# Kernel optimization log

Measured on AMD Instinct MI355X. Metric: run time of the kernel, lower is better.

Reference implementation:

```python
import jax, jax.numpy as jnp
import numpy as np

S, B, C, H, W = 5, 2, 128, 24, 24
N_ITER = 3
BN_EPS = 1e-5


def conv2d(x, w, b, pad):
    # x: (N, Cin, H, W), w: (Cout, Cin, kh, kw)
    y = jax.lax.conv_general_dilated(
        x, w, (1, 1), [(pad, pad), (pad, pad)],
        dimension_numbers=('NCHW', 'OIHW', 'NCHW'))
    return y + b[None, :, None, None]


def setup_inputs() -> dict:
    key = jax.random.key(0)
    ks = jax.random.split(key, 8)
    sc = 0.03  # keep pre-softmax logits in a sane range
    d = {}
    d['x'] = jax.random.normal(ks[0], (S, B, C, H, W), jnp.float32) * 0.5
    d['Wf_w'] = jax.random.normal(ks[1], (C, C, 3, 3), jnp.float32) * sc
    d['Wf_b'] = jnp.zeros((C,), jnp.float32)
    d['Wh_w'] = jax.random.normal(ks[2], (C, C, 3, 3), jnp.float32) * sc
    d['Wh_b'] = jnp.zeros((C,), jnp.float32)
    d['Wl_w'] = jax.random.normal(ks[3], (C, C, 3, 3), jnp.float32) * sc
    d['Wl_b'] = jnp.zeros((C,), jnp.float32)
    d['alpha'] = jnp.ones((1,), jnp.float32)
    d['Wc'] = jax.random.normal(ks[4], (C, C), jnp.float32) * sc
    d['Wg_w'] = jax.random.normal(ks[5], (C, C, 3, 3), jnp.float32) * sc
    d['Wg_b'] = jnp.zeros((C,), jnp.float32)
    d['bn_gamma'] = jnp.ones((C,), jnp.float32)
    d['bn_beta'] = jnp.zeros((C,), jnp.float32)
    d['gru_zr_w'] = jax.random.normal(ks[6], (2 * C, 2 * C, 5, 5), jnp.float32) * sc
    d['gru_zr_b'] = jnp.zeros((2 * C,), jnp.float32)
    d['gru_h_w'] = jax.random.normal(ks[7], (C, 2 * C, 5, 5), jnp.float32) * sc
    d['gru_h_b'] = jnp.zeros((C,), jnp.float32)
    d['intra_w'] = jnp.full((1,), 0.5, jnp.float32)
    d['inter_w'] = jnp.full((1,), 0.5, jnp.float32)
    return d


def reference(x, Wf_w, Wf_b, Wh_w, Wh_b, Wl_w, Wl_b, alpha, Wc, Wg_w, Wg_b,
              bn_gamma, bn_beta, gru_zr_w, gru_zr_b, gru_h_w, gru_h_b,
              intra_w, inter_w):
    S_, B_, C_, H_, W_ = x.shape
    N = H_ * W_
    # BatchNorm2d in inference mode with fresh running stats (mean=0, var=1)
    bn_scale = bn_gamma / jnp.sqrt(1.0 + BN_EPS)
    mask = (1.0 - jnp.eye(S_, dtype=x.dtype))[:, :, None, None, None, None]
    h = x
    for _ in range(N_ITER):
        hb = h.reshape(S_ * B_, C_, H_, W_)
        # ---- intra-node self-attention (per node in sequence) ----
        ft = conv2d(hb, Wf_w, Wf_b, 1).reshape(S_, B_, C_, N)
        ht = conv2d(hb, Wh_w, Wh_b, 1).reshape(S_, B_, C_, N)
        lt = conv2d(hb, Wl_w, Wl_b, 1).reshape(S_, B_, C_, N)
        att = jax.nn.softmax(jnp.einsum('sbcn,sbcm->sbnm', ft, ht), axis=-1)
        ctx = jnp.einsum('sbnm,sbcm->sbcn', att, lt).reshape(S_, B_, C_, H_, W_)
        eii = alpha[0] * ctx + h
        # ---- inter-node pairwise attention messages (all i,j pairs) ----
        hf = h.reshape(S_, B_, C_, N)
        yt = jnp.einsum('cd,jbdn->jbcn', Wc, hf)
        eij = jnp.einsum('ibcn,jbcm->ijbnm', hf, yt)  # (S,S,B,N,N)
        eijn = jax.nn.softmax(eij, axis=-1)
        mji = jnp.einsum('ijbnm,jbcm->ijbcn', eijn, hf)  # (S,S,B,C,N)
        m4 = mji.reshape(S_ * S_ * B_, C_, H_, W_)
        g = jax.nn.sigmoid(jnp.mean(conv2d(m4, Wg_w, Wg_b, 1),
                                    axis=(2, 3), keepdims=True))
        mg = (g * m4) * bn_scale[None, :, None, None] + bn_beta[None, :, None, None]
        mg = mg.reshape(S_, S_, B_, C_, H_, W_)
        inter = jnp.sum(mg * mask, axis=1)  # exclude j == i
        msg = intra_w[0] * eii + inter_w[0] * inter
        # ---- ConvGRU update + residual ----
        xi = msg.reshape(S_ * B_, C_, H_, W_)
        zr = jax.nn.sigmoid(conv2d(jnp.concatenate([xi, hb], axis=1),
                                   gru_zr_w, gru_zr_b, 2))
        z, r = zr[:, :C_], zr[:, C_:]
        h_hat = jnp.tanh(conv2d(jnp.concatenate([xi, r * hb], axis=1),
                                gru_h_w, gru_h_b, 2))
        h_new = (1.0 - z) * hb + z * h_hat
        h = (h_new + hb).reshape(S_, B_, C_, H_, W_)
    return h
```

## Files before the change

kernel.cpp:

```cpp
#include <hip/hip_runtime.h>
#include <math.h>

#define S_  5
#define B_  2
#define C_  128
#define N_  576
#define SB  10
#define NPAIR 40
#define C2  256

typedef short v8s __attribute__((ext_vector_type(8)));
typedef float v4f __attribute__((ext_vector_type(4)));

#define GLOBAL_AS __attribute__((address_space(1)))
#define LDS_AS    __attribute__((address_space(3)))

__device__ __forceinline__ unsigned short f2bf(float f) {
    union { float f; unsigned u; } v; v.f = f;
    unsigned r = (v.u + 0x7FFF + ((v.u >> 16) & 1)) >> 16;
    return (unsigned short)r;
}
__device__ __forceinline__ float bf2f(unsigned short h) {
    union { unsigned u; float f; } v; v.u = ((unsigned)h) << 16;
    return v.f;
}

__global__ void packA5_kernel(const float* __restrict__ w, unsigned short* __restrict__ Apk, int M)
{
    int idx = blockIdx.x * 256 + threadIdx.x;
    if (idx >= M * 6400) return;
    int r = idx;
    int j = r & 7;      r >>= 3;
    int quad = r & 3;   r >>= 2;
    int l15 = r & 15;   r >>= 4;
    int c = r & 3;      r >>= 2;
    int tap_l = r % 5;  r /= 5;
    int g = r % 5;      r /= 5;
    int ch = r & 1;     r >>= 1;
    int kk = r & 3;     r >>= 2;
    int cgb = r;
    int co = cgb * 64 + c * 16 + l15;
    int ci = kk * 64 + ch * 32 + quad * 8 + j;
    int tap = g * 5 + tap_l;
    Apk[idx] = f2bf(w[((size_t)co * 256 + ci) * 25 + tap]);
}
__global__ void packA3_kernel(const float* __restrict__ wf, const float* __restrict__ wh,
                              const float* __restrict__ wl, unsigned short* __restrict__ Apk)
{
    int idx = blockIdx.x * 256 + threadIdx.x;
    if (idx >= 384 * 1152) return;
    int r = idx;
    int j = r & 7;      r >>= 3;
    int quad = r & 3;   r >>= 2;
    int l15 = r & 15;   r >>= 4;
    int c = r & 3;      r >>= 2;
    int tap_l = r % 3;  r /= 3;
    int g = r % 3;      r /= 3;
    int ch = r & 1;     r >>= 1;
    int kk = r & 1;     r >>= 1;
    int cgb = r;
    int co = cgb * 64 + c * 16 + l15;
    const float* w = (co < 128) ? wf : (co < 256) ? wh : wl;
    int cl = co & 127;
    int ci = kk * 64 + ch * 32 + quad * 8 + j;
    int tap = g * 3 + tap_l;
    Apk[idx] = f2bf(w[((size_t)cl * 128 + ci) * 9 + tap]);
}
__global__ void packWc_kernel(const float* __restrict__ w, unsigned short* __restrict__ o)
{
    int idx = blockIdx.x * 256 + threadIdx.x;
    if (idx < 128 * 128) o[idx] = f2bf(w[idx]);
}
__global__ void packWgT_kernel(const float* __restrict__ w, float* __restrict__ o)
{
    int idx = blockIdx.x * 256 + threadIdx.x;
    if (idx >= 128 * 1152) return;
    int co = idx & 127, i = idx >> 7;
    o[(size_t)i * 128 + co] = w[(size_t)co * 1152 + i];
}

__global__ __launch_bounds__(256) void tc_kernel(
    const float* __restrict__ src, const float* __restrict__ zrp,
    const float* __restrict__ zrb,
    unsigned short* __restrict__ dst, unsigned short* __restrict__ vfd)
{
    const size_t PLANE = (size_t)SB * C2 * N_;
    __shared__ float tile[128][9];
    int img = blockIdx.y, px0 = blockIdx.x * 8, t = threadIdx.x;
    #pragma unroll
    for (int i = 0; i < 4; ++i) {
        int e = i * 256 + t; int ci = e >> 3; int px = e & 7;
        float v = src[((size_t)img * 128 + ci) * 576 + px0 + px];
        if (zrp) {
            size_t zi = ((size_t)img * C2 + 128 + ci) * 576 + px0 + px;
            float a = zrb[128 + ci];
            #pragma unroll
            for (int k = 0; k < 4; ++k) a += zrp[k * PLANE + zi];
            v *= 1.f / (1.f + __expf(-a));
        }
        tile[ci][px] = v;
        if (vfd) {
            int m = px0 + px;
            int ctile = ci >> 4, l15v = ci & 15;
            int sIdx = m >> 5, quadv = (m >> 3) & 3, j = m & 7;
            vfd[(((size_t)img * 8 + ctile) * 18 + sIdx) * 512 + (quadv * 16 + l15v) * 8 + j] = f2bf(v);
        }
    }
    __syncthreads();
    #pragma unroll
    for (int i = 0; i < 4; ++i) {
        int e = i * 256 + t; int pxl = e >> 7; int ci = e & 127;
        dst[((size_t)img * 576 + px0 + pxl) * 128 + ci] = f2bf(tile[ci][pxl]);
    }
}

template<int KD, int R, int CINT, int SPLITK, int MODE>
__global__ __launch_bounds__(256, 1) void conv_mfma(
    const unsigned short* __restrict__ srcA, const unsigned short* __restrict__ srcB,
    const unsigned short* __restrict__ Apk, int COUT, float* __restrict__ po,
    const float* __restrict__ b0, const float* __restrict__ b1, const float* __restrict__ b2,
    unsigned short* __restrict__ t0, unsigned short* __restrict__ t1,
    unsigned short* __restrict__ t2)
{
    constexpr int PART   = CINT / SPLITK;
    constexpr int NCH    = PART / 32;
    constexpr int NSUB   = NCH * KD;
    constexpr int WR     = 8 + 2 * R;
    constexpr int WC     = 24 + 2 * R;
    constexpr int NPOS   = WR * WC;
    constexpr int NSLOTB = NPOS * 4;
    constexpr int RB     = (NSLOTB + 255) / 256;
    constexpr int AUNITS = KD * 4 * 64;
    constexpr int AR     = AUNITS / 256;
    __shared__ __align__(16) unsigned short Ab[2][AUNITS * 8];
    __shared__ __align__(16) unsigned short Bb[NPOS * 32];

    int f   = blockIdx.x;
    int kk  = f % SPLITK;
    int cgb = f / SPLITK;
    int pxb = blockIdx.y;
    int img = blockIdx.z;
    int t = threadIdx.x;
    int wave = t >> 6, lane = t & 63;
    int quad = lane >> 4, l15 = lane & 15;
    int r0 = pxb * 8;

    const int cibase = kk * PART;
    const unsigned short* src = (cibase >= 128) ? srcB : srcA;
    const int cioff0 = cibase & 127;
    const unsigned short* srcI = src + (size_t)img * 576 * 128;

    int posBase[3], pxs[3];
    #pragma unroll
    for (int s = 0; s < 3; ++s) {
        int px = pxb * 192 + wave * 48 + s * 16 + l15;
        pxs[s] = px;
        int pr = px / 24, pc = px % 24;
        posBase[s] = (pr - r0 + R) * WC + pc + R;
    }

    int goffB[RB]; bool gokB[RB];
    #pragma unroll
    for (int rr = 0; rr < RB; ++rr) {
        int idx = rr * 256 + wave * 64 + lane;
        int pos = idx >> 2, slotq = idx & 3;
        int gr = slotq ^ ((pos >> 1) & 3);
        int wr = pos / WC, wc = pos % WC;
        int grow = r0 - R + wr, gcol = wc - R;
        gokB[rr] = (idx < NSLOTB) && grow >= 0 && grow < 24 && gcol >= 0 && gcol < 24;
        goffB[rr] = (grow * 24 + gcol) * 128 + gr * 8;
    }

    auto stageB = [&](int ch) {
        const unsigned short* sp = srcI + cioff0 + ch * 32;
        #pragma unroll
        for (int rr = 0; rr < RB; ++rr) {
            if (gokB[rr]) {
                __builtin_amdgcn_global_load_lds(
                    (const GLOBAL_AS void*)(sp + goffB[rr]),
                    (LDS_AS void*)((char*)&Bb[0] + (size_t)(rr * 256 + wave * 64) * 16),
                    16, 0, 0);
            }
        }
    };
    auto stageA = [&](int sub, int buf) {
        const unsigned short* sp = Apk + ((size_t)((cgb * SPLITK + kk) * NSUB + sub)) * (AUNITS * 8);
        #pragma unroll
        for (int r = 0; r < AR; ++r) {
            int u0 = r * 256 + wave * 64;
            __builtin_amdgcn_global_load_lds(
                (const GLOBAL_AS void*)(sp + (size_t)(u0 + lane) * 8),
                (LDS_AS void*)((char*)&Ab[buf][0] + (size_t)u0 * 16),
                16, 0, 0);
        }
    };

    v4f acc[4][3];
    #pragma unroll
    for (int c = 0; c < 4; ++c)
        #pragma unroll
        for (int s = 0; s < 3; ++s)
            #pragma unroll
            for (int r = 0; r < 4; ++r) acc[c][s][r] = 0.f;

    {
        v8s zv;
        #pragma unroll
        for (int j = 0; j < 8; ++j) zv[j] = 0;
        for (int i = t; i < NPOS * 4; i += 256) ((v8s*)Bb)[i] = zv;
    }
    __syncthreads();
    stageB(0);
    stageA(0, 0);
    __syncthreads();

    int sub = 0;
    #pragma unroll 1
    for (int ch = 0; ch < NCH; ++ch) {
        #pragma unroll 1
        for (int g = 0; g < KD; ++g) {
            if (sub + 1 < NSUB) stageA(sub + 1, (sub + 1) & 1);
            const unsigned short* Ap = &Ab[sub & 1][0];
            #pragma unroll
            for (int tl = 0; tl < KD; ++tl) {
                int doff = (g - R) * WC + (tl - R);
                v8s a[4];
                #pragma unroll
                for (int c = 0; c < 4; ++c)
                    a[c] = *(const v8s*)&Ap[((tl * 4 + c) * 64 + l15 * 4 + quad) * 8];
                v8s b[3];
                #pragma unroll
                for (int s = 0; s < 3; ++s) {
                    int pos = posBase[s] + doff;
                    b[s] = *(const v8s*)&Bb[pos * 32 + ((quad ^ ((pos >> 1) & 3)) << 3)];
                }
                #pragma unroll
                for (int c = 0; c < 4; ++c)
                    #pragma unroll
                    for (int s = 0; s < 3; ++s)
                        acc[c][s] = __builtin_amdgcn_mfma_f32_16x16x32_bf16(a[c], b[s], acc[c][s], 0, 0, 0);
            }
            __syncthreads();
            ++sub;
        }
        if (ch + 1 < NCH) { stageB(ch + 1); __syncthreads(); }
    }

    if (MODE == 0) {
        float* out = po + (size_t)kk * ((size_t)SB * COUT * 576)
                   + ((size_t)img * COUT + cgb * 64) * 576;
        #pragma unroll
        for (int c = 0; c < 4; ++c)
            #pragma unroll
            for (int s = 0; s < 3; ++s)
                #pragma unroll
                for (int r = 0; r < 4; ++r) {
                    int col = c * 16 + quad * 4 + r;
                    out[(size_t)col * 576 + pxs[s]] = acc[c][s][r];
                }
    } else {
        #pragma unroll
        for (int c = 0; c < 4; ++c)
            #pragma unroll
            for (int s = 0; s < 3; ++s) {
                int px = pxs[s];
                #pragma unroll
                for (int r = 0; r < 4; ++r) {
                    int co = cgb * 64 + c * 16 + quad * 4 + r;
                    int which = co >> 7, cl = co & 127;
                    const float* bp = (which == 0) ? b0 : (which == 1) ? b1 : b2;
                    float v = acc[c][s][r] + bp[cl];
                    if (which == 0) {
                        t0[((size_t)img * 576 + px) * 128 + cl] = f2bf(v);
                    } else if (which == 1) {
                        int mt = px >> 4, l15m = px & 15;
                        int kb = cl >> 5, quadk = (cl >> 3) & 3, jj = cl & 7;
                        t1[(((size_t)img * 36 + mt) * 4 + kb) * 512 + (quadk * 16 + l15m) * 8 + jj] = f2bf(v);
                    } else {
                        int ctile = cl >> 4, l15v = cl & 15;
                        int sIdx = px >> 5, quadv = (px >> 3) & 3, jj = px & 7;
                        t2[(((size_t)img * 8 + ctile) * 18 + sIdx) * 512 + (quadv * 16 + l15v) * 8 + jj] = f2bf(v);
                    }
                }
            }
    }
}

__global__ __launch_bounds__(256) void yt_mfma(
    const unsigned short* __restrict__ hT, const unsigned short* __restrict__ Wcb,
    unsigned short* __restrict__ KFi)
{
    int t = threadIdx.x, wave = t >> 6, lane = t & 63;
    int q = lane >> 4, l15 = lane & 15;
    int n0 = blockIdx.x * 16, img = blockIdx.y;
    v4f acc[2];
    #pragma unroll
    for (int ct = 0; ct < 2; ++ct)
        #pragma unroll
        for (int r = 0; r < 4; ++r) acc[ct][r] = 0.f;
    #pragma unroll
    for (int kk = 0; kk < 4; ++kk) {
        v8s b = *(const v8s*)(hT + ((size_t)img * 576 + n0 + l15) * 128 + kk * 32 + q * 8);
        #pragma unroll
        for (int ct = 0; ct < 2; ++ct) {
            v8s a = *(const v8s*)(Wcb + (size_t)((wave * 2 + ct) * 16 + l15) * 128 + kk * 32 + q * 8);
            acc[ct] = __builtin_amdgcn_mfma_f32_16x16x32_bf16(a, b, acc[ct], 0, 0, 0);
        }
    }
    int mt = blockIdx.x;
    #pragma unroll
    for (int ct = 0; ct < 2; ++ct) {
        #pragma unroll
        for (int r = 0; r < 4; ++r) {
            int co = (wave * 2 + ct) * 16 + q * 4 + r;
            int kk = co >> 5, quadk = (co >> 3) & 3, j = co & 7;
            KFi[(((size_t)img * 36 + mt) * 4 + kk) * 512 + (quadk * 16 + l15) * 8 + j]
                = f2bf(acc[ct][r]);
        }
    }
}

template<int MODE>
__global__ __launch_bounds__(256) void attn_mfma(
    const unsigned short* __restrict__ QT, const unsigned short* __restrict__ KF,
    const unsigned short* __restrict__ VF, float* __restrict__ Of,
    unsigned short* __restrict__ Oh, const float* __restrict__ addsrc,
    const float* __restrict__ alpha)
{
    __shared__ __align__(16) unsigned short P[16 * 576];
    __shared__ float redmx[4][16];
    __shared__ float redsm[4][16];
    int t = threadIdx.x;
    int wave = t >> 6, lane = t & 63;
    int q = lane >> 4, l15 = lane & 15;
    int n0 = blockIdx.x * 16;
    int p = blockIdx.y;
    int qimg, kimg;
    if (MODE == 0) { qimg = p; kimg = p; }
    else {
        int b = p & 1; int ij = p >> 1; int i = ij >> 2; int jj = ij & 3;
        int j = jj + (jj >= i ? 1 : 0);
        qimg = i * 2 + b; kimg = j * 2 + b;
    }
    const unsigned short* Qp = QT + ((size_t)qimg * 576 + n0) * 128;
    const unsigned short* Kp = KF + (size_t)kimg * 36 * 4 * 512;
    const unsigned short* Vp = VF + (size_t)kimg * 8 * 18 * 512;

    v8s aq[4];
    #pragma unroll
    for (int kk = 0; kk < 4; ++kk)
        aq[kk] = *(const v8s*)(Qp + (size_t)l15 * 128 + kk * 32 + q * 8);

    v4f S[9];
    #pragma unroll
    for (int i = 0; i < 9; ++i)
        #pragma unroll
        for (int r = 0; r < 4; ++r) S[i][r] = 0.f;

    #pragma unroll
    for (int i = 0; i < 9; ++i) {
        int mt = wave * 9 + i;
        #pragma unroll
        for (int kk = 0; kk < 4; ++kk) {
            v8s b = *(const v8s*)(Kp + ((size_t)(mt * 4 + kk)) * 512 + lane * 8);
            S[i] = __builtin_amdgcn_mfma_f32_16x16x32_bf16(aq[kk], b, S[i], 0, 0, 0);
        }
    }

    float mx[4];
    #pragma unroll
    for (int r = 0; r < 4; ++r) {
        float m = S[0][r];
        #pragma unroll
        for (int i = 1; i < 9; ++i) m = fmaxf(m, S[i][r]);
        #pragma unroll
        for (int off = 1; off < 16; off <<= 1) m = fmaxf(m, __shfl_xor(m, off));
        mx[r] = m;
    }
    if (l15 == 0) {
        #pragma unroll
        for (int r = 0; r < 4; ++r) redmx[wave][q * 4 + r] = mx[r];
    }
    __syncthreads();
    float sum[4];
    #pragma unroll
    for (int r = 0; r < 4; ++r) {
        float g = fmaxf(fmaxf(redmx[0][q * 4 + r], redmx[1][q * 4 + r]),
                        fmaxf(redmx[2][q * 4 + r], redmx[3][q * 4 + r]));
        float s = 0.f;
        #pragma unroll
        for (int i = 0; i < 9; ++i) { float e = __expf(S[i][r] - g); S[i][r] = e; s += e; }
        #pragma unroll
        for (int off = 1; off < 16; off <<= 1) s += __shfl_xor(s, off);
        sum[r] = s;
    }
    if (l15 == 0) {
        #pragma unroll
        for (int r = 0; r < 4; ++r) redsm[wave][q * 4 + r] = sum[r];
    }
    #pragma unroll
    for (int i = 0; i < 9; ++i) {
        int m = (wave * 9 + i) * 16 + l15;
        int cm = m >> 3, mo = m & 7;
        #pragma unroll
        for (int r = 0; r < 4; ++r) {
            int n = q * 4 + r;
            P[n * 576 + ((cm ^ (n & 7)) << 3) + mo] = f2bf(S[i][r]);
        }
    }
    __syncthreads();
    float inv[4];
    #pragma unroll
    for (int r = 0; r < 4; ++r)
        inv[r] = 1.f / (redsm[0][q * 4 + r] + redsm[1][q * 4 + r] +
                        redsm[2][q * 4 + r] + redsm[3][q * 4 + r]);

    v4f o[2];
    #pragma unroll
    for (int ct = 0; ct < 2; ++ct)
        #pragma unroll
        for (int r = 0; r < 4; ++r) o[ct][r] = 0.f;

    for (int s = 0; s < 18; ++s) {
        int cm = s * 4 + q;
        v8s a = *(const v8s*)&P[l15 * 576 + ((cm ^ (l15 & 7)) << 3)];
        #pragma unroll
        for (int ct = 0; ct < 2; ++ct) {
            int ctile = wave * 2 + ct;
            v8s b = *(const v8s*)(Vp + ((size_t)(ctile * 18 + s)) * 512 + lane * 8);
            o[ct] = __builtin_amdgcn_mfma_f32_16x16x32_bf16(a, b, o[ct], 0, 0, 0);
        }
    }

    #pragma unroll
    for (int ct = 0; ct < 2; ++ct) {
        int c = (wave * 2 + ct) * 16 + l15;
        size_t base = ((size_t)p * 128 + c) * 576 + n0 + q * 4;
        if (MODE == 0) {
            float al = alpha[0];
            #pragma unroll
            for (int r = 0; r < 4; ++r)
                Of[base + r] = al * o[ct][r] * inv[r] + addsrc[base + r];
        } else {
            #pragma unroll
            for (int r = 0; r < 4; ++r)
                Oh[base + r] = f2bf(o[ct][r] * inv[r]);
        }
    }
}

__global__ __launch_bounds__(64) void wsum_kernel(
    const unsigned short* __restrict__ mji, float* __restrict__ wsum)
{
    int pair = blockIdx.x, ci = blockIdx.y, lane = threadIdx.x;
    const unsigned short* p = mji + ((size_t)pair * C_ + ci) * N_;
    float T=0, R0=0, R23=0, Cl=0, Cr=0, c00=0, c0w=0, ch0=0, chw=0;
    for (int i = lane; i < N_; i += 64) {
        float v = bf2f(p[i]);
        int r = i / 24, cc = i % 24;
        T += v;
        if (r == 0)  R0  += v;
        if (r == 23) R23 += v;
        if (cc == 0)  Cl += v;
        if (cc == 23) Cr += v;
        if (i == 0)   c00 = v;
        if (i == 23)  c0w = v;
        if (i == 552) ch0 = v;
        if (i == 575) chw = v;
    }
    #pragma unroll
    for (int off = 32; off > 0; off >>= 1) {
        T  += __shfl_xor(T, off);  R0 += __shfl_xor(R0, off);  R23 += __shfl_xor(R23, off);
        Cl += __shfl_xor(Cl, off); Cr += __shfl_xor(Cr, off);
        c00 += __shfl_xor(c00, off); c0w += __shfl_xor(c0w, off);
        ch0 += __shfl_xor(ch0, off); chw += __shfl_xor(chw, off);
    }
    if (lane == 0) {
        float rowsub[3] = {R23, 0.f, R0};
        float colsub[3] = {Cr,  0.f, Cl};
        float corner[9] = {chw, 0.f, ch0,  0.f, 0.f, 0.f,  c0w, 0.f, c00};
        float* o = wsum + ((size_t)pair * C_ + ci) * 9;
        #pragma unroll
        for (int ky = 0; ky < 3; ++ky)
            #pragma unroll
            for (int kx = 0; kx < 3; ++kx)
                o[ky * 3 + kx] = T - rowsub[ky] - colsub[kx] + corner[ky * 3 + kx];
    }
}

__global__ __launch_bounds__(128) void g_kernel(
    const float* __restrict__ wsum, const float* __restrict__ WgT,
    const float* __restrict__ Wgb, float* __restrict__ g)
{
    __shared__ float sw[C_ * 9];
    int pair = blockIdx.x; int co = threadIdx.x;
    for (int i = co; i < C_ * 9; i += 128) sw[i] = wsum[(size_t)pair * C_ * 9 + i];
    __syncthreads();
    float acc = 0.f;
    for (int i = 0; i < C_ * 9; ++i) acc += WgT[(size_t)i * 128 + co] * sw[i];
    float m = acc * (1.f / 576.f) + Wgb[co];
    g[pair * C_ + co] = 1.f / (1.f + __expf(-m));
}

__global__ __launch_bounds__(256) void msg_tc_kernel(
    const float* __restrict__ eii, const unsigned short* __restrict__ mji,
    const float* __restrict__ g, const float* __restrict__ bn_gamma,
    const float* __restrict__ bn_beta, const float* __restrict__ intra_w,
    const float* __restrict__ inter_w, unsigned short* __restrict__ msgT)
{
    __shared__ float tile[128][9];
    int img = blockIdx.y, px0 = blockIdx.x * 8, t = threadIdx.x;
    int s = img >> 1, b = img & 1;
    float iw = intra_w[0], ew = inter_w[0];
    #pragma unroll
    for (int i = 0; i < 4; ++i) {
        int e = i * 256 + t; int ci = e >> 3; int pxl = e & 7;
        int px = px0 + pxl;
        float scale = bn_gamma[ci] * rsqrtf(1.f + 1e-5f);
        float acc = 0.f;
        #pragma unroll
        for (int jj = 0; jj < 4; ++jj) {
            int pidx = (s * 4 + jj) * 2 + b;
            acc += g[pidx * C_ + ci] * bf2f(mji[((size_t)pidx * C_ + ci) * N_ + px]);
        }
        float inter = scale * acc + 4.f * bn_beta[ci];
        tile[ci][pxl] = iw * eii[((size_t)img * C_ + ci) * N_ + px] + ew * inter;
    }
    __syncthreads();
    #pragma unroll
    for (int i = 0; i < 4; ++i) {
        int e = i * 256 + t; int pxl = e >> 7; int ci = e & 127;
        msgT[((size_t)img * 576 + px0 + pxl) * 128 + ci] = f2bf(tile[ci][pxl]);
    }
}

__global__ __launch_bounds__(256) void update_tc_kernel(
    const float* __restrict__ zrp, const float* __restrict__ zrb,
    const float* __restrict__ hhp, const float* __restrict__ ghb,
    const float* __restrict__ h, float* __restrict__ out,
    unsigned short* __restrict__ hTn, unsigned short* __restrict__ VFn, int last)
{
    const size_t ZP = (size_t)SB * C2 * N_;
    const size_t HP = (size_t)SB * C_ * N_;
    __shared__ float tile[128][9];
    int img = blockIdx.y, px0 = blockIdx.x * 8, t = threadIdx.x;
    #pragma unroll
    for (int i = 0; i < 4; ++i) {
        int e = i * 256 + t; int ci = e >> 3; int pxl = e & 7;
        int px = px0 + pxl;
        size_t zi = ((size_t)img * C2 + ci) * N_ + px;
        float za = zrb[ci];
        #pragma unroll
        for (int k = 0; k < 4; ++k) za += zrp[k * ZP + zi];
        float z = 1.f / (1.f + __expf(-za));
        size_t hi = ((size_t)img * C_ + ci) * N_ + px;
        float ha = ghb[ci];
        #pragma unroll
        for (int k = 0; k < 4; ++k) ha += hhp[k * HP + hi];
        float hh = tanhf(ha);
        float o = (2.f - z) * h[hi] + z * hh;
        out[hi] = o;
        tile[ci][pxl] = o;
        if (!last) {
            int ctile = ci >> 4, l15v = ci & 15;
            int sIdx = px >> 5, quadv = (px >> 3) & 3, j = px & 7;
            VFn[(((size_t)img * 8 + ctile) * 18 + sIdx) * 512 + (quadv * 16 + l15v) * 8 + j] = f2bf(o);
        }
    }
    if (!last) {
        __syncthreads();
        #pragma unroll
        for (int i = 0; i < 4; ++i) {
            int e = i * 256 + t; int pxl = e >> 7; int ci = e & 127;
            hTn[((size_t)img * 576 + px0 + pxl) * 128 + ci] = f2bf(tile[ci][pxl]);
        }
    }
}

extern "C" void kernel_launch(void* const* d_in, const int* in_sizes, int n_in,
                              void* d_out, int out_size, void* d_ws, size_t ws_size,
                              hipStream_t stream)
{
    const float* x      = (const float*)d_in[0];
    const float* Wf_w   = (const float*)d_in[1];
    const float* Wf_b   = (const float*)d_in[2];
    const float* Wh_w   = (const float*)d_in[3];
    const float* Wh_b   = (const float*)d_in[4];
    const float* Wl_w   = (const float*)d_in[5];
    const float* Wl_b   = (const float*)d_in[6];
    const float* alpha  = (const float*)d_in[7];
    const float* Wc     = (const float*)d_in[8];
    const float* Wg_w   = (const float*)d_in[9];
    const float* Wg_b   = (const float*)d_in[10];
    const float* bng    = (const float*)d_in[11];
    const float* bnb    = (const float*)d_in[12];
    const float* zr_w   = (const float*)d_in[13];
    const float* zr_b   = (const float*)d_in[14];
    const float* gh_w   = (const float*)d_in[15];
    const float* gh_b   = (const float*)d_in[16];
    const float* intraw = (const float*)d_in[17];
    const float* interw = (const float*)d_in[18];
    float* outp = (float*)d_out;

    float* f = (float*)d_ws;
    const size_t SZ = (size_t)SB * C_ * N_;
    float* hbuf  = f; f += SZ;
    float* eii   = f; f += SZ;
    float* zrp   = f; f += 4 * (size_t)SB * C2 * N_;
    float* hhp   = f; f += 4 * SZ;
    float* wsumb = f; f += (size_t)NPAIR * C_ * 9;
    float* gbuf  = f; f += (size_t)NPAIR * C_;
    float* WgT   = f; f += (size_t)128 * 1152;
    unsigned short* us = (unsigned short*)f;
    unsigned short* mji16  = us; us += (size_t)NPAIR * C_ * N_;
    unsigned short* hT16   = us; us += SZ;
    unsigned short* hc16   = us; us += SZ;
    unsigned short* msgT16 = us; us += SZ;
    unsigned short* ftT    = us; us += SZ;
    unsigned short* KFa    = us; us += SZ;
    unsigned short* VFa    = us; us += SZ;
    unsigned short* Wp3    = us; us += (size_t)384 * 1152;
    unsigned short* Wpzr   = us; us += (size_t)256 * 6400;
    unsigned short* Wph    = us; us += (size_t)128 * 6400;
    unsigned short* Wcb    = us; us += (size_t)128 * 128;

    unsigned short* KFi    = ftT;
    unsigned short* VFi    = hc16;
    unsigned short* rhbT16 = hc16;

    packA3_kernel<<<(384 * 1152 + 255) / 256, 256, 0, stream>>>(Wf_w, Wh_w, Wl_w, Wp3);
    packA5_kernel<<<(256 * 6400 + 255) / 256, 256, 0, stream>>>(zr_w, Wpzr, 256);
    packA5_kernel<<<(128 * 6400 + 255) / 256, 256, 0, stream>>>(gh_w, Wph, 128);
    packWc_kernel<<<64, 256, 0, stream>>>(Wc, Wcb);
    packWgT_kernel<<<(128 * 1152 + 255) / 256, 256, 0, stream>>>(Wg_w, WgT);

    tc_kernel<<<dim3(72, SB), 256, 0, stream>>>(x, nullptr, nullptr, hT16, VFi);

    const float* hcur = x;
    for (int it = 0; it < 3; ++it) {
        float* hout = (it == 2) ? outp : hbuf;

        conv_mfma<3, 1, 128, 1, 1><<<dim3(6, 3, SB), 256, 0, stream>>>(
            hT16, hT16, Wp3, 384, nullptr, Wf_b, Wh_b, Wl_b, ftT, KFa, VFa);
        attn_mfma<0><<<dim3(36, SB), 256, 0, stream>>>(ftT, KFa, VFa, eii, nullptr, hcur, alpha);
        yt_mfma<<<dim3(36, SB), 256, 0, stream>>>(hT16, Wcb, KFi);
        attn_mfma<1><<<dim3(36, NPAIR), 256, 0, stream>>>(hT16, KFi, VFi, nullptr, mji16, nullptr, nullptr);
        wsum_kernel<<<dim3(NPAIR, C_), 64, 0, stream>>>(mji16, wsumb);
        g_kernel<<<NPAIR, 128, 0, stream>>>(wsumb, WgT, Wg_b, gbuf);
        msg_tc_kernel<<<dim3(72, SB), 256, 0, stream>>>(eii, mji16, gbuf, bng, bnb, intraw, interw, msgT16);
        conv_mfma<5, 2, 256, 4, 0><<<dim3(16, 3, SB), 256, 0, stream>>>(
            msgT16, hT16, Wpzr, 256, zrp, nullptr, nullptr, nullptr, nullptr, nullptr, nullptr);
        tc_kernel<<<dim3(72, SB), 256, 0, stream>>>(hcur, zrp, zr_b, rhbT16, nullptr);
        conv_mfma<5, 2, 256, 4, 0><<<dim3(8, 3, SB), 256, 0, stream>>>(
            msgT16, rhbT16, Wph, 128, hhp, nullptr, nullptr, nullptr, nullptr, nullptr, nullptr);
        update_tc_kernel<<<dim3(72, SB), 256, 0, stream>>>(
            zrp, zr_b, hhp, gh_b, hcur, hout, hT16, VFi, (it == 2) ? 1 : 0);
        hcur = hout;
    }
}
```

Baseline: 615.4 us.

## Process 32 query rows per attention block to reuse V fragments

The attention kernel now handles 32 query rows per block instead of 16. Each wave computes scores for one 16-row query tile over half of the keys, and the softmax max and sum are reduced across wave pairs. In the PV stage, each V fragment loaded from global memory feeds two MFMAs, one per query tile, which halves V traffic per output. The cost is twice the score registers per wave (18 accumulators), twice the LDS for P, and half as many blocks, so occupancy and parallelism drop.

New measurement: 643.5 us. 4.6% more time.

```diff
diff --git a/kernel.cpp b/kernel.cpp
--- a/kernel.cpp
+++ b/kernel.cpp
@@ -327,13 +327,14 @@
     unsigned short* __restrict__ Oh, const float* __restrict__ addsrc,
     const float* __restrict__ alpha)
 {
-    __shared__ __align__(16) unsigned short P[16 * 576];
-    __shared__ float redmx[4][16];
-    __shared__ float redsm[4][16];
+    __shared__ __align__(16) unsigned short P[32 * 576];
+    __shared__ float redmx[2][2][16];
+    __shared__ float redsm[2][2][16];
     int t = threadIdx.x;
     int wave = t >> 6, lane = t & 63;
     int q = lane >> 4, l15 = lane & 15;
-    int n0 = blockIdx.x * 16;
+    int qt = wave & 1, mhalf = wave >> 1;
+    int n0 = blockIdx.x * 32;
     int p = blockIdx.y;
     int qimg, kimg;
     if (MODE == 0) { qimg = p; kimg = p; }
@@ -342,7 +343,7 @@
         int j = jj + (jj >= i ? 1 : 0);
         qimg = i * 2 + b; kimg = j * 2 + b;
     }
-    const unsigned short* Qp = QT + ((size_t)qimg * 576 + n0) * 128;
+    const unsigned short* Qp = QT + ((size_t)qimg * 576 + n0 + qt * 16) * 128;
     const unsigned short* Kp = KF + (size_t)kimg * 36 * 4 * 512;
     const unsigned short* Vp = VF + (size_t)kimg * 8 * 18 * 512;
 
@@ -351,15 +352,15 @@
     for (int kk = 0; kk < 4; ++kk)
         aq[kk] = *(const v8s*)(Qp + (size_t)l15 * 128 + kk * 32 + q * 8);
 
-    v4f S[9];
-    #pragma unroll
-    for (int i = 0; i < 9; ++i)
+    v4f S[18];
+    #pragma unroll
+    for (int i = 0; i < 18; ++i)
         #pragma unroll
         for (int r = 0; r < 4; ++r) S[i][r] = 0.f;
 
     #pragma unroll
-    for (int i = 0; i < 9; ++i) {
-        int mt = wave * 9 + i;
+    for (int i = 0; i < 18; ++i) {
+        int mt = mhalf * 18 + i;
         #pragma unroll
         for (int kk = 0; kk < 4; ++kk) {
             v8s b = *(const v8s*)(Kp + ((size_t)(mt * 4 + kk)) * 512 + lane * 8);
@@ -372,79 +373,81 @@
     for (int r = 0; r < 4; ++r) {
         float m = S[0][r];
         #pragma unroll
-        for (int i = 1; i < 9; ++i) m = fmaxf(m, S[i][r]);
+        for (int i = 1; i < 18; ++i) m = fmaxf(m, S[i][r]);
         #pragma unroll
         for (int off = 1; off < 16; off <<= 1) m = fmaxf(m, __shfl_xor(m, off));
         mx[r] = m;
     }
     if (l15 == 0) {
         #pragma unroll
-        for (int r = 0; r < 4; ++r) redmx[wave][q * 4 + r] = mx[r];
+        for (int r = 0; r < 4; ++r) redmx[qt][mhalf][q * 4 + r] = mx[r];
     }
     __syncthreads();
-    float sum[4];
     #pragma unroll
     for (int r = 0; r < 4; ++r) {
-        float g = fmaxf(fmaxf(redmx[0][q * 4 + r], redmx[1][q * 4 + r]),
-                        fmaxf(redmx[2][q * 4 + r], redmx[3][q * 4 + r]));
+        float g = fmaxf(redmx[qt][0][q * 4 + r], redmx[qt][1][q * 4 + r]);
         float s = 0.f;
         #pragma unroll
-        for (int i = 0; i < 9; ++i) { float e = __expf(S[i][r] - g); S[i][r] = e; s += e; }
+        for (int i = 0; i < 18; ++i) { float e = __expf(S[i][r] - g); S[i][r] = e; s += e; }
         #pragma unroll
         for (int off = 1; off < 16; off <<= 1) s += __shfl_xor(s, off);
-        sum[r] = s;
-    }
-    if (l15 == 0) {
-        #pragma unroll
-        for (int r = 0; r < 4; ++r) redsm[wave][q * 4 + r] = sum[r];
-    }
-    #pragma unroll
-    for (int i = 0; i < 9; ++i) {
-        int m = (wave * 9 + i) * 16 + l15;
+        if (l15 == 0) redsm[qt][mhalf][q * 4 + r] = s;
+    }
+    #pragma unroll
+    for (int i = 0; i < 18; ++i) {
+        int m = (mhalf * 18 + i) * 16 + l15;
         int cm = m >> 3, mo = m & 7;
         #pragma unroll
         for (int r = 0; r < 4; ++r) {
-            int n = q * 4 + r;
+            int n = qt * 16 + q * 4 + r;
             P[n * 576 + ((cm ^ (n & 7)) << 3) + mo] = f2bf(S[i][r]);
         }
     }
     __syncthreads();
-    float inv[4];
-    #pragma unroll
-    for (int r = 0; r < 4; ++r)
-        inv[r] = 1.f / (redsm[0][q * 4 + r] + redsm[1][q * 4 + r] +
-                        redsm[2][q * 4 + r] + redsm[3][q * 4 + r]);
-
-    v4f o[2];
+    float inv2[2][4];
+    #pragma unroll
+    for (int q2 = 0; q2 < 2; ++q2)
+        #pragma unroll
+        for (int r = 0; r < 4; ++r)
+            inv2[q2][r] = 1.f / (redsm[q2][0][q * 4 + r] + redsm[q2][1][q * 4 + r]);
+
+    v4f o[2][2];
     #pragma unroll
     for (int ct = 0; ct < 2; ++ct)
         #pragma unroll
-        for (int r = 0; r < 4; ++r) o[ct][r] = 0.f;
+        for (int q2 = 0; q2 < 2; ++q2)
+            #pragma unroll
+            for (int r = 0; r < 4; ++r) o[ct][q2][r] = 0.f;
 
     for (int s = 0; s < 18; ++s) {
         int cm = s * 4 + q;
-        v8s a = *(const v8s*)&P[l15 * 576 + ((cm ^ (l15 & 7)) << 3)];
+        v8s a0 = *(const v8s*)&P[(0 * 16 + l15) * 576 + ((cm ^ (l15 & 7)) << 3)];
+        v8s a1 = *(const v8s*)&P[(1 * 16 + l15) * 576 + ((cm ^ (l15 & 7)) << 3)];
         #pragma unroll
         for (int ct = 0; ct < 2; ++ct) {
             int ctile = wave * 2 + ct;
             v8s b = *(const v8s*)(Vp + ((size_t)(ctile * 18 + s)) * 512 + lane * 8);
-            o[ct] = __builtin_amdgcn_mfma_f32_16x16x32_bf16(a, b, o[ct], 0, 0, 0);
+            o[ct][0] = __builtin_amdgcn_mfma_f32_16x16x32_bf16(a0, b, o[ct][0], 0, 0, 0);
+            o[ct][1] = __builtin_amdgcn_mfma_f32_16x16x32_bf16(a1, b, o[ct][1], 0, 0, 0);
         }
     }
 
     #pragma unroll
     for (int ct = 0; ct < 2; ++ct) {
         int c = (wave * 2 + ct) * 16 + l15;
-        size_t base = ((size_t)p * 128 + c) * 576 + n0 + q * 4;
-        if (MODE == 0) {
-            float al = alpha[0];
-            #pragma unroll
-            for (int r = 0; r < 4; ++r)
-                Of[base + r] = al * o[ct][r] * inv[r] + addsrc[base + r];
-        } else {
-            #pragma unroll
-            for (int r = 0; r < 4; ++r)
-                Oh[base + r] = f2bf(o[ct][r] * inv[r]);
+        #pragma unroll
+        for (int q2 = 0; q2 < 2; ++q2) {
+            size_t base = ((size_t)p * 128 + c) * 576 + n0 + q2 * 16 + q * 4;
+            if (MODE == 0) {
+                float al = alpha[0];
+                #pragma unroll
+                for (int r = 0; r < 4; ++r)
+                    Of[base + r] = al * o[ct][q2][r] * inv2[q2][r] + addsrc[base + r];
+            } else {
+                #pragma unroll
+                for (int r = 0; r < 4; ++r)
+                    Oh[base + r] = f2bf(o[ct][q2][r] * inv2[q2][r]);
+            }
         }
     }
 }
@@ -642,9 +645,9 @@
 
         conv_mfma<3, 1, 128, 1, 1><<<dim3(6, 3, SB), 256, 0, stream>>>(
             hT16, hT16, Wp3, 384, nullptr, Wf_b, Wh_b, Wl_b, ftT, KFa, VFa);
-        attn_mfma<0><<<dim3(36, SB), 256, 0, stream>>>(ftT, KFa, VFa, eii, nullptr, hcur, alpha);
+        attn_mfma<0><<<dim3(18, SB), 256, 0, stream>>>(ftT, KFa, VFa, eii, nullptr, hcur, alpha);
         yt_mfma<<<dim3(36, SB), 256, 0, stream>>>(hT16, Wcb, KFi);
-        attn_mfma<1><<<dim3(36, NPAIR), 256, 0, stream>>>(hT16, KFi, VFi, nullptr, mji16, nullptr, nullptr);
+        attn_mfma<1><<<dim3(18, NPAIR), 256, 0, stream>>>(hT16, KFi, VFi, nullptr, mji16, nullptr, nullptr);
         wsum_kernel<<<dim3(NPAIR, C_), 64, 0, stream>>>(mji16, wsumb);
         g_kernel<<<NPAIR, 128, 0, stream>>>(wsumb, WgT, Wg_b, gbuf);
         msg_tc_kernel<<<dim3(72, SB), 256, 0, stream>>>(eii, mji16, gbuf, bng, bnb, intraw, interw, msgT16);
```
